# Optimization experiments

Measured on AMD Instinct MI355X. Metric: run time of the kernel, lower is better.

Reference implementation:

```python
import jax, jax.numpy as jnp
import numpy as np
from jax import lax

T, B, D, H = 512, 64, 256, 512  # time, batch, input_dim, hidden_dim


def setup_inputs() -> dict:
    key = jax.random.key(0)
    ks = jax.random.split(key, 9)
    fan_in = D + H
    s = 1.0 / np.sqrt(fan_in)
    inputs = jax.random.normal(ks[0], (T, B, D), dtype=jnp.float32)
    # torch nn.Linear weight layout: [out_features, in_features]
    Wf = jax.random.uniform(ks[1], (H, fan_in), jnp.float32, -s, s)
    bf = jax.random.uniform(ks[2], (H,), jnp.float32, -s, s)
    Wi = jax.random.uniform(ks[3], (H, fan_in), jnp.float32, -s, s)
    bi = jax.random.uniform(ks[4], (H,), jnp.float32, -s, s)
    Wg = jax.random.uniform(ks[5], (H, fan_in), jnp.float32, -s, s)
    bg = jax.random.uniform(ks[6], (H,), jnp.float32, -s, s)
    Wo = jax.random.uniform(ks[7], (H, fan_in), jnp.float32, -s, s)
    bo = jax.random.uniform(ks[8], (H,), jnp.float32, -s, s)
    return {"inputs": inputs, "Wf": Wf, "bf": bf, "Wi": Wi, "bi": bi,
            "Wg": Wg, "bg": bg, "Wo": Wo, "bo": bo}


def reference(inputs, Wf, bf, Wi, bi, Wg, bg, Wo, bo):
    # LSTM-style gated recurrence, n_qubits=0 path (no depth loop, proj_back = Identity)
    batch = inputs.shape[1]
    hidden = bf.shape[0]
    h0 = jnp.zeros((batch, hidden), inputs.dtype)
    c0 = jnp.zeros((batch, hidden), inputs.dtype)

    def step(carry, x):
        hx, cx = carry
        comb = jnp.concatenate([x, hx], axis=1)  # [B, D+H]
        f = jax.nn.sigmoid(comb @ Wf.T + bf)
        i = jax.nn.sigmoid(comb @ Wi.T + bi)
        g = jnp.tanh(comb @ Wg.T + bg)
        o = jax.nn.sigmoid(comb @ Wo.T + bo)
        cx = f * cx + i * g
        hx = o * jnp.tanh(cx)
        return (hx, cx), hx

    (hx, cx), outputs = lax.scan(step, (h0, c0), inputs)
    return outputs, hx, cx
```

## Files before the change

### kernel.cpp

```cpp
#include <hip/hip_runtime.h>
#include <stdint.h>

#define T_STEPS 512
#define BATCH   64
#define DIN     256
#define HID     512
#define KTOT    768
#define NTEAMS  4
#define TB      16
#define KK_X    8
#define KK_H    16
#define KK_ALL  24

#define POLL_BOUND (1 << 18)
#define DET_BOUND  (1 << 20)

typedef __bf16 v8bf __attribute__((ext_vector_type(8)));
typedef float  v4f  __attribute__((ext_vector_type(4)));
typedef unsigned int v4u __attribute__((ext_vector_type(4)));
typedef unsigned int v2u __attribute__((ext_vector_type(2)));

#define FLAGS_OFF 0
#define XCDB_OFF  8192
#define XCNT_OFF  8704
#define WPK_OFF   16384
#define XPK_OFF   (WPK_OFF + 3145728)
#define HBUF_OFF  (XPK_OFF + 16777216)
#define WS_NEED   ((size_t)HBUF_OFF + 33554432u)
#define FLAGS5_OFF 0
#define HBUF5_OFF  8192
#define WPK5_OFF   (HBUF5_OFF + 131072)
#define XPK5_OFF   (WPK5_OFF + 3145728)

#define LOADX4_DEV(d, a, IMM) \
  asm volatile("global_load_dwordx4 %0, %1, off offset:" IMM " sc1" \
               : "=v"(d) : "v"(a) : "memory")
#define LOADX4_PLAIN(d, a, IMM) \
  asm volatile("global_load_dwordx4 %0, %1, off offset:" IMM \
               : "=v"(d) : "v"(a) : "memory")
#define ST2_DEV(a, v) \
  asm volatile("global_store_dwordx2 %0, %1, off sc1" :: "v"(a), "v"(v) : "memory")
#define ST2_PLAIN(a, v) \
  asm volatile("global_store_dwordx2 %0, %1, off" :: "v"(a), "v"(v) : "memory")
#define ST_DW_DEV(a, v) \
  asm volatile("global_store_dword %0, %1, off sc1" :: "v"(a), "v"(v) : "memory")
#define ST_DW_SYS(a, v) \
  asm volatile("global_store_dword %0, %1, off sc0 sc1" :: "v"(a), "v"(v) : "memory")
#define LOADX4(d, a) \
  asm volatile("global_load_dwordx4 %0, %1, off" : "=v"(d) : "v"(a) : "memory")
#define LOAD_DW_NB(d, a) \
  asm volatile("global_load_dword %0, %1, off sc1" : "=v"(d) : "v"(a) : "memory")
#define WAIT1() asm volatile("s_waitcnt vmcnt(1)" ::: "memory")
#define DRAIN_VM() asm volatile("s_waitcnt vmcnt(0)" ::: "memory")

static __device__ __forceinline__ unsigned int ld_flag_dev(const unsigned int* p) {
  unsigned int v;
  asm volatile("global_load_dword %0, %1, off sc1\n\ts_waitcnt vmcnt(0)"
               : "=v"(v) : "v"(p) : "memory");
  return v;
}
static __device__ __forceinline__ unsigned int ld_dword_sys(const unsigned int* p) {
  unsigned int v;
  asm volatile("global_load_dword %0, %1, off sc0 sc1\n\ts_waitcnt vmcnt(0)"
               : "=v"(v) : "v"(p) : "memory");
  return v;
}

static __device__ __forceinline__ unsigned short f2bf(float x) {
  union { float f; uint32_t u; } v; v.f = x;
  uint32_t r = (v.u + 0x7fffu + ((v.u >> 16) & 1u)) >> 16;
  return (unsigned short)r;
}
static __device__ __forceinline__ float sigm(float x) {
  float e = __builtin_amdgcn_exp2f(-1.44269504f * x);
  return __builtin_amdgcn_rcpf(1.0f + e);
}
static __device__ __forceinline__ float tanh_(float x) {
  float e = __builtin_amdgcn_exp2f(2.88539008f * x);
  return 1.0f - 2.0f * __builtin_amdgcn_rcpf(e + 1.0f);
}

__global__ void pack_w(const float* __restrict__ Wf, const float* __restrict__ Wi,
                       const float* __restrict__ Wg, const float* __restrict__ Wo,
                       unsigned short* __restrict__ wpk) {
  int n = blockIdx.x * 256 + threadIdx.x;
  int l  = n & 63;
  int kk = (n >> 6) % KK_ALL;
  int wv = (n >> 6) / KK_ALL;
  int row  = l & 15;
  int gate = row & 3;
  int unit = (wv >> 2) * 16 + (wv & 3) * 4 + (row >> 2);
  int col  = kk * 32 + (l >> 4) * 8;
  const float* W = (gate == 0) ? Wf : (gate == 1) ? Wi : (gate == 2) ? Wg : Wo;
  const float* src = W + (size_t)unit * KTOT + col;
  unsigned short* dst = wpk + (size_t)n * 8;
#pragma unroll
  for (int e = 0; e < 8; e++) dst[e] = f2bf(src[e]);
}

__global__ void pack_x(const float* __restrict__ X, unsigned short* __restrict__ xpk) {
  int n = blockIdx.x * 256 + threadIdx.x;
  int l    = n & 63;
  int kk   = (n >> 6) & 7;
  int team = (n >> 9) & 3;
  int t    = n >> 11;
  int b    = team * TB + (l & 15);
  int col  = kk * 32 + (l >> 4) * 8;
  const float* src = X + ((size_t)(t * BATCH + b)) * DIN + col;
  unsigned short* dst = xpk + (size_t)n * 8;
#pragma unroll
  for (int e = 0; e < 8; e++) dst[e] = f2bf(src[e]);
}

__global__ void __launch_bounds__(256, 1)
lstm_mono(const float* __restrict__ bf_, const float* __restrict__ bi_,
          const float* __restrict__ bg_, const float* __restrict__ bo_,
          const unsigned short* __restrict__ wpk, const unsigned short* __restrict__ xpk,
          float* __restrict__ out, unsigned int* flags, unsigned int* xcdb,
          unsigned int* xcnt, unsigned short* hbuf) {
  int blk  = blockIdx.x;
  int team = blk & 7;
  if (team >= NTEAMS) return;
  int cu  = blk >> 3;
  int tid = threadIdx.x;
  int w   = tid >> 6, l = tid & 63;
  int brow = l & 15;
  int ul   = l >> 4;
  int u    = cu * 16 + w * 4 + ul;
  int bglob = team * TB + brow;

  __shared__ v4u hls[2048];
  __shared__ int mode_sh;

  {
    unsigned int* xb = xcdb + team * 32;
    unsigned int* xc = xcnt + team * 16;
    if (w == 0) {
      if (l == 0) {
        unsigned int myx;
        asm volatile("s_getreg_b32 %0, hwreg(HW_REG_XCC_ID)" : "=s"(myx));
        ST_DW_SYS(xb + cu, myx + 1u);
        DRAIN_VM();
        __hip_atomic_fetch_add(xc, 1u, __ATOMIC_RELEASE, __HIP_MEMORY_SCOPE_AGENT);
        int guard = 0;
        while (__hip_atomic_load(xc, __ATOMIC_ACQUIRE, __HIP_MEMORY_SCOPE_AGENT) < 32u) {
          if (++guard > DET_BOUND) break;
        }
      }
      unsigned int xv = ld_dword_sys(xb + (l & 31));
      int ok = (__all(xv == __shfl(xv, 0)) && __shfl(xv, 0) != 0u) ? 1 : 0;
      if (l == 0) mode_sh = ok;
    }
    __syncthreads();
  }
  const int fastsc = mode_sh;

  v4u wfu[KK_ALL];
  {
    const char* wp = (const char*)(wpk + ((size_t)(cu * 4 + w)) * (KK_ALL * 512) + l * 8);
#pragma unroll
    for (int kk = 0; kk < KK_ALL; kk++) LOADX4(wfu[kk], wp + (size_t)kk * 1024);
    DRAIN_VM();
  }
  float b0 = bf_[u], b1 = bi_[u], b2 = bg_[u], b3 = bo_[u];
  float c = 0.0f, hval = 0.0f;

  unsigned int* ftm = flags + (size_t)team * 32 * 16;
  unsigned int* myflag = ftm + (size_t)cu * 16;

  float* outb = out + (size_t)bglob * HID + u;

  for (int t = 0; t < T_STEPS; t++) {
    v8bf xf[KK_X];
    {
      const v8bf* xp = (const v8bf*)(xpk + ((size_t)(t * NTEAMS + team)) * (KK_X * 512) + l * 8);
#pragma unroll
      for (int kk = 0; kk < KK_X; kk++) xf[kk] = xp[kk * 64];
    }

    v4f acc[4];
    acc[0] = (v4f){b0, b1, b2, b3};
    acc[1] = (v4f){0.f, 0.f, 0.f, 0.f};
    acc[2] = (v4f){0.f, 0.f, 0.f, 0.f};
    acc[3] = (v4f){0.f, 0.f, 0.f, 0.f};
#pragma unroll
    for (int kk = 0; kk < KK_X; kk++)
      acc[kk & 3] = __builtin_amdgcn_mfma_f32_16x16x32_bf16(
          __builtin_bit_cast(v8bf, wfu[kk]), xf[kk], acc[kk & 3], 0, 0, 0);

    if (t > 0) {
      if (w == 0) {
        const unsigned int* pp = ftm + (size_t)(l & 31) * 16;
        unsigned int tg = (unsigned)t;
        unsigned int fa, fb;
        LOAD_DW_NB(fa, pp);
        int guard = 0;
        while (true) {
          LOAD_DW_NB(fb, pp);
          WAIT1();
          __builtin_amdgcn_sched_barrier(0);
          if (__all(fa >= tg)) break;
          LOAD_DW_NB(fa, pp);
          WAIT1();
          __builtin_amdgcn_sched_barrier(0);
          if (__all(fb >= tg)) break;
          if ((guard += 2) > POLL_BOUND) break;
        }
      }
      __syncthreads();

      const char* slab_t = (const char*)(hbuf + ((size_t)t * NTEAMS + team) * (TB * HID));
      const char* sb = slab_t + w * 4096 + l * 16;
      v4u s0, s1, s2, s3;
      if (fastsc) {
        LOADX4_PLAIN(s0, sb, "0");
        LOADX4_PLAIN(s1, sb, "1024");
        LOADX4_PLAIN(s2, sb, "2048");
        LOADX4_PLAIN(s3, sb, "3072");
      } else {
        LOADX4_DEV(s0, sb, "0");
        LOADX4_DEV(s1, sb, "1024");
        LOADX4_DEV(s2, sb, "2048");
        LOADX4_DEV(s3, sb, "3072");
      }
      DRAIN_VM();
      __builtin_amdgcn_sched_barrier(0);

      char* hl = (char*)hls + (t & 1) * 16384;
      {
        int r = w * 4;
        *(v4u*)(hl + (((r + 0) * 1024 + l * 16) ^ (((r + 0) & 7) << 4))) = s0;
        *(v4u*)(hl + (((r + 1) * 1024 + l * 16) ^ (((r + 1) & 7) << 4))) = s1;
        *(v4u*)(hl + (((r + 2) * 1024 + l * 16) ^ (((r + 2) & 7) << 4))) = s2;
        *(v4u*)(hl + (((r + 3) * 1024 + l * 16) ^ (((r + 3) & 7) << 4))) = s3;
      }
      __syncthreads();

#pragma unroll
      for (int kk = 0; kk < KK_H; kk++) {
        int off = (brow * 1024 + kk * 64 + ul * 16) ^ ((brow & 7) << 4);
        v8bf hf = *(const v8bf*)(hl + off);
        acc[kk & 3] = __builtin_amdgcn_mfma_f32_16x16x32_bf16(
            __builtin_bit_cast(v8bf, wfu[KK_X + kk]), hf, acc[kk & 3], 0, 0, 0);
      }
    }

    v4f g4 = (acc[0] + acc[1]) + (acc[2] + acc[3]);
    float fg = sigm(g4[0]);
    float ig = sigm(g4[1]);
    float gg = tanh_(g4[2]);
    float og = sigm(g4[3]);
    c    = fg * c + ig * gg;
    hval = og * tanh_(c);

    if (t < T_STEPS - 1) {
      float h0 = __shfl(hval, brow);
      float h1 = __shfl(hval, brow + 16);
      float h2 = __shfl(hval, brow + 32);
      float h3 = __shfl(hval, brow + 48);
      char* slab_n = (char*)(hbuf + ((size_t)(t + 1) * NTEAMS + team) * (TB * HID));
      if (l < 16) {
        v2u pk;
        pk.x = (unsigned)f2bf(h0) | ((unsigned)f2bf(h1) << 16);
        pk.y = (unsigned)f2bf(h2) | ((unsigned)f2bf(h3) << 16);
        char* pd = slab_n + brow * 1024 + cu * 32 + w * 8;
        if (fastsc) { ST2_PLAIN(pd, pk); } else { ST2_DEV(pd, pk); }
      }
      outb[(size_t)t * (BATCH * HID)] = hval;
      DRAIN_VM();
      __syncthreads();
      if (tid == 0) ST_DW_DEV(myflag, (unsigned)(t + 1));
    } else {
      outb[(size_t)t * (BATCH * HID)] = hval;
    }
  }

  float* hx = out + (size_t)T_STEPS * BATCH * HID;
  hx[(size_t)bglob * HID + u] = hval;
  float* cx = hx + BATCH * HID;
  cx[(size_t)bglob * HID + u] = c;
}

__global__ void __launch_bounds__(256, 1)
lstm_rec_r5(const float* __restrict__ bf_, const float* __restrict__ bi_,
            const float* __restrict__ bg_, const float* __restrict__ bo_,
            const unsigned short* __restrict__ wpk, const unsigned short* __restrict__ xpk,
            float* __restrict__ out, unsigned int* flags, unsigned short* hbuf) {
  int blk  = blockIdx.x;
  int team = blk & 7;
  if (team >= NTEAMS) return;
  int cu  = blk >> 3;
  int tid = threadIdx.x;
  int w   = tid >> 6, l = tid & 63;
  int brow = l & 15;
  int ul   = l >> 4;
  int u    = cu * 16 + w * 4 + ul;
  int bglob = team * TB + brow;

  __shared__ v4u hls[1024];
  char* hl = (char*)hls;

  v4u wfu[KK_ALL];
  {
    const char* wp = (const char*)(wpk + ((size_t)(cu * 4 + w)) * (KK_ALL * 512) + l * 8);
#pragma unroll
    for (int kk = 0; kk < KK_ALL; kk++) LOADX4(wfu[kk], wp + (size_t)kk * 1024);
    DRAIN_VM();
  }
  float b0 = bf_[u], b1 = bi_[u], b2 = bg_[u], b3 = bo_[u];
  float c = 0.0f, hval = 0.0f;

  char* slab0 = (char*)(hbuf + (size_t)team * 2 * (TB * HID));
  char* slab1 = slab0 + TB * HID * 2;
  unsigned int* ftm = flags + (size_t)team * 32 * 16;
  unsigned int* myflag = ftm + (size_t)cu * 16;
  float* outb = out + (size_t)bglob * HID + u;

  for (int t = 0; t < T_STEPS; t++) {
    v8bf xf[KK_X];
    {
      const v8bf* xp = (const v8bf*)(xpk + ((size_t)(t * NTEAMS + team)) * (KK_X * 512) + l * 8);
#pragma unroll
      for (int kk = 0; kk < KK_X; kk++) xf[kk] = xp[kk * 64];
    }
    if (t > 0) {
      if (w == 0) {
        const unsigned int* pp = ftm + (size_t)(l & 31) * 16;
        int guard = 0;
        while (true) {
          unsigned int v = ld_flag_dev(pp);
          if (__all(v >= (unsigned)t)) break;
          if (++guard > POLL_BOUND) break;
        }
      }
      __syncthreads();
    }
    v4u s0, s1, s2, s3;
    {
      const char* sb = ((t & 1) ? slab1 : slab0) + w * 4096 + l * 16;
      LOADX4_DEV(s0, sb, "0");
      LOADX4_DEV(s1, sb, "1024");
      LOADX4_DEV(s2, sb, "2048");
      LOADX4_DEV(s3, sb, "3072");
    }
    v4f acc[4];
    acc[0] = (v4f){b0, b1, b2, b3};
    acc[1] = (v4f){0.f, 0.f, 0.f, 0.f};
    acc[2] = (v4f){0.f, 0.f, 0.f, 0.f};
    acc[3] = (v4f){0.f, 0.f, 0.f, 0.f};
#pragma unroll
    for (int kk = 0; kk < KK_X; kk++)
      acc[kk & 3] = __builtin_amdgcn_mfma_f32_16x16x32_bf16(
          __builtin_bit_cast(v8bf, wfu[kk]), xf[kk], acc[kk & 3], 0, 0, 0);
    DRAIN_VM();
    __builtin_amdgcn_sched_barrier(0);
    {
      int r = w * 4;
      *(v4u*)(hl + (((r + 0) * 1024 + l * 16) ^ (((r + 0) & 7) << 4))) = s0;
      *(v4u*)(hl + (((r + 1) * 1024 + l * 16) ^ (((r + 1) & 7) << 4))) = s1;
      *(v4u*)(hl + (((r + 2) * 1024 + l * 16) ^ (((r + 2) & 7) << 4))) = s2;
      *(v4u*)(hl + (((r + 3) * 1024 + l * 16) ^ (((r + 3) & 7) << 4))) = s3;
    }
    __syncthreads();
#pragma unroll
    for (int kk = 0; kk < KK_H; kk++) {
      int off = (brow * 1024 + kk * 64 + ul * 16) ^ ((brow & 7) << 4);
      v8bf hf = *(const v8bf*)(hl + off);
      acc[kk & 3] = __builtin_amdgcn_mfma_f32_16x16x32_bf16(
          __builtin_bit_cast(v8bf, wfu[KK_X + kk]), hf, acc[kk & 3], 0, 0, 0);
    }
    v4f g4 = (acc[0] + acc[1]) + (acc[2] + acc[3]);
    float fg = sigm(g4[0]);
    float ig = sigm(g4[1]);
    float gg = tanh_(g4[2]);
    float og = sigm(g4[3]);
    c    = fg * c + ig * gg;
    hval = og * tanh_(c);
    if (t < T_STEPS - 1) {
      float h0 = __shfl(hval, brow);
      float h1 = __shfl(hval, brow + 16);
      float h2 = __shfl(hval, brow + 32);
      float h3 = __shfl(hval, brow + 48);
      if (l < 16) {
        v2u pk;
        pk.x = (unsigned)f2bf(h0) | ((unsigned)f2bf(h1) << 16);
        pk.y = (unsigned)f2bf(h2) | ((unsigned)f2bf(h3) << 16);
        char* pd = (((t + 1) & 1) ? slab1 : slab0) + brow * 1024 + cu * 32 + w * 8;
        ST2_DEV(pd, pk);
      }
      DRAIN_VM();
      __syncthreads();
      if (tid == 0) ST_DW_DEV(myflag, (unsigned)(t + 1));
    }
    outb[(size_t)t * (BATCH * HID)] = hval;
  }
  float* hx = out + (size_t)T_STEPS * BATCH * HID;
  hx[(size_t)bglob * HID + u] = hval;
  float* cx = hx + BATCH * HID;
  cx[(size_t)bglob * HID + u] = c;
}

extern "C" void kernel_launch(void* const* d_in, const int* in_sizes, int n_in,
                              void* d_out, int out_size, void* d_ws, size_t ws_size,
                              hipStream_t stream) {
  const float* X  = (const float*)d_in[0];
  const float* Wf = (const float*)d_in[1];
  const float* bf = (const float*)d_in[2];
  const float* Wi = (const float*)d_in[3];
  const float* bi = (const float*)d_in[4];
  const float* Wg = (const float*)d_in[5];
  const float* bg = (const float*)d_in[6];
  const float* Wo = (const float*)d_in[7];
  const float* bo = (const float*)d_in[8];
  float* out = (float*)d_out;
  char* ws = (char*)d_ws;

  if (ws_size >= WS_NEED) {
    unsigned int*   flags = (unsigned int*)(ws + FLAGS_OFF);
    unsigned int*   xcdb  = (unsigned int*)(ws + XCDB_OFF);
    unsigned int*   xcnt  = (unsigned int*)(ws + XCNT_OFF);
    unsigned short* wpk   = (unsigned short*)(ws + WPK_OFF);
    unsigned short* xpk   = (unsigned short*)(ws + XPK_OFF);
    unsigned short* hbuf  = (unsigned short*)(ws + HBUF_OFF);
    hipMemsetAsync(ws, 0, WPK_OFF, stream);
    pack_w<<<768, 256, 0, stream>>>(Wf, Wi, Wg, Wo, wpk);
    pack_x<<<4096, 256, 0, stream>>>(X, xpk);
    lstm_mono<<<256, 256, 0, stream>>>(bf, bi, bg, bo, wpk, xpk, out,
                                       flags, xcdb, xcnt, hbuf);
  } else {
    unsigned int*   flags = (unsigned int*)(ws + FLAGS5_OFF);
    unsigned short* hbuf  = (unsigned short*)(ws + HBUF5_OFF);
    unsigned short* wpk   = (unsigned short*)(ws + WPK5_OFF);
    unsigned short* xpk   = (unsigned short*)(ws + XPK5_OFF);
    hipMemsetAsync(ws, 0, WPK5_OFF, stream);
    pack_w<<<768, 256, 0, stream>>>(Wf, Wi, Wg, Wo, wpk);
    pack_x<<<4096, 256, 0, stream>>>(X, xpk);
    lstm_rec_r5<<<256, 256, 0, stream>>>(bf, bi, bg, bo, wpk, xpk, out, flags, hbuf);
  }
}
```

Before: 1.631 ms.

## Embed step tags in hidden-state words to replace flag polling with speculative loads

Each bf16 hidden value is now stored in a 32-bit word whose low 16 bits carry the step number. Readers issue the h loads speculatively before the x-part MFMAs, then check the tags and fall back to flag polling only if any word is stale. The h buffer becomes a 64-slot ring. The XCC-detection prologue and the plain-cache fast path are dropped in favour of device-scope loads and stores. This targets the poll-then-load round trip and the barrier on each step, at the cost of doubling the h traffic and relying on 16-byte stores being observed atomically.

```diff
diff --git a/kernel.cpp b/kernel.cpp
--- a/kernel.cpp
+++ b/kernel.cpp
@@ -13,7 +13,6 @@
 #define KK_ALL  24
 
 #define POLL_BOUND (1 << 18)
-#define DET_BOUND  (1 << 20)
 
 typedef __bf16 v8bf __attribute__((ext_vector_type(8)));
 typedef float  v4f  __attribute__((ext_vector_type(4)));
@@ -21,12 +20,10 @@
 typedef unsigned int v2u __attribute__((ext_vector_type(2)));
 
 #define FLAGS_OFF 0
-#define XCDB_OFF  8192
-#define XCNT_OFF  8704
 #define WPK_OFF   16384
 #define XPK_OFF   (WPK_OFF + 3145728)
-#define HBUF_OFF  (XPK_OFF + 16777216)
-#define WS_NEED   ((size_t)HBUF_OFF + 33554432u)
+#define HB32_OFF  (XPK_OFF + 16777216)
+#define WS_NEED   ((size_t)HB32_OFF + 8388608u)
 #define FLAGS5_OFF 0
 #define HBUF5_OFF  8192
 #define WPK5_OFF   (HBUF5_OFF + 131072)
@@ -35,33 +32,19 @@
 #define LOADX4_DEV(d, a, IMM) \
   asm volatile("global_load_dwordx4 %0, %1, off offset:" IMM " sc1" \
                : "=v"(d) : "v"(a) : "memory")
-#define LOADX4_PLAIN(d, a, IMM) \
-  asm volatile("global_load_dwordx4 %0, %1, off offset:" IMM \
-               : "=v"(d) : "v"(a) : "memory")
+#define ST4_DEV(a, v) \
+  asm volatile("global_store_dwordx4 %0, %1, off sc1" :: "v"(a), "v"(v) : "memory")
 #define ST2_DEV(a, v) \
   asm volatile("global_store_dwordx2 %0, %1, off sc1" :: "v"(a), "v"(v) : "memory")
-#define ST2_PLAIN(a, v) \
-  asm volatile("global_store_dwordx2 %0, %1, off" :: "v"(a), "v"(v) : "memory")
 #define ST_DW_DEV(a, v) \
   asm volatile("global_store_dword %0, %1, off sc1" :: "v"(a), "v"(v) : "memory")
-#define ST_DW_SYS(a, v) \
-  asm volatile("global_store_dword %0, %1, off sc0 sc1" :: "v"(a), "v"(v) : "memory")
 #define LOADX4(d, a) \
   asm volatile("global_load_dwordx4 %0, %1, off" : "=v"(d) : "v"(a) : "memory")
-#define LOAD_DW_NB(d, a) \
-  asm volatile("global_load_dword %0, %1, off sc1" : "=v"(d) : "v"(a) : "memory")
-#define WAIT1() asm volatile("s_waitcnt vmcnt(1)" ::: "memory")
 #define DRAIN_VM() asm volatile("s_waitcnt vmcnt(0)" ::: "memory")
 
 static __device__ __forceinline__ unsigned int ld_flag_dev(const unsigned int* p) {
   unsigned int v;
   asm volatile("global_load_dword %0, %1, off sc1\n\ts_waitcnt vmcnt(0)"
-               : "=v"(v) : "v"(p) : "memory");
-  return v;
-}
-static __device__ __forceinline__ unsigned int ld_dword_sys(const unsigned int* p) {
-  unsigned int v;
-  asm volatile("global_load_dword %0, %1, off sc0 sc1\n\ts_waitcnt vmcnt(0)"
                : "=v"(v) : "v"(p) : "memory");
   return v;
 }
@@ -113,11 +96,10 @@
 }
 
 __global__ void __launch_bounds__(256, 1)
-lstm_mono(const float* __restrict__ bf_, const float* __restrict__ bi_,
+lstm_spec(const float* __restrict__ bf_, const float* __restrict__ bi_,
           const float* __restrict__ bg_, const float* __restrict__ bo_,
           const unsigned short* __restrict__ wpk, const unsigned short* __restrict__ xpk,
-          float* __restrict__ out, unsigned int* flags, unsigned int* xcdb,
-          unsigned int* xcnt, unsigned short* hbuf) {
+          float* __restrict__ out, unsigned int* flags, unsigned int* hb32) {
   int blk  = blockIdx.x;
   int team = blk & 7;
   if (team >= NTEAMS) return;
@@ -130,30 +112,6 @@
   int bglob = team * TB + brow;
 
   __shared__ v4u hls[2048];
-  __shared__ int mode_sh;
-
-  {
-    unsigned int* xb = xcdb + team * 32;
-    unsigned int* xc = xcnt + team * 16;
-    if (w == 0) {
-      if (l == 0) {
-        unsigned int myx;
-        asm volatile("s_getreg_b32 %0, hwreg(HW_REG_XCC_ID)" : "=s"(myx));
-        ST_DW_SYS(xb + cu, myx + 1u);
-        DRAIN_VM();
-        __hip_atomic_fetch_add(xc, 1u, __ATOMIC_RELEASE, __HIP_MEMORY_SCOPE_AGENT);
-        int guard = 0;
-        while (__hip_atomic_load(xc, __ATOMIC_ACQUIRE, __HIP_MEMORY_SCOPE_AGENT) < 32u) {
-          if (++guard > DET_BOUND) break;
-        }
-      }
-      unsigned int xv = ld_dword_sys(xb + (l & 31));
-      int ok = (__all(xv == __shfl(xv, 0)) && __shfl(xv, 0) != 0u) ? 1 : 0;
-      if (l == 0) mode_sh = ok;
-    }
-    __syncthreads();
-  }
-  const int fastsc = mode_sh;
 
   v4u wfu[KK_ALL];
   {
@@ -168,16 +126,31 @@
   unsigned int* ftm = flags + (size_t)team * 32 * 16;
   unsigned int* myflag = ftm + (size_t)cu * 16;
 
+  int r    = w * 4 + (l >> 4);
+  int scol = l & 15;
+
   float* outb = out + (size_t)bglob * HID + u;
+  const unsigned int SEL = 0x07060302u;
 
   for (int t = 0; t < T_STEPS; t++) {
+    char* slab_t = (char*)(hb32 + ((size_t)(t & 63) * NTEAMS + team) * (TB * HID));
+    char* slab_n = (char*)(hb32 + ((size_t)((t + 1) & 63) * NTEAMS + team) * (TB * HID));
+
+    v4u p0, p1, p2, p3, p4, p5, p6, p7;
+    const char* sb = slab_t + r * 2048 + scol * 32;
+    if (t > 0) {
+      LOADX4_DEV(p0, sb, "0");    LOADX4_DEV(p1, sb, "16");
+      LOADX4_DEV(p2, sb, "512");  LOADX4_DEV(p3, sb, "528");
+      LOADX4_DEV(p4, sb, "1024"); LOADX4_DEV(p5, sb, "1040");
+      LOADX4_DEV(p6, sb, "1536"); LOADX4_DEV(p7, sb, "1552");
+    }
+
     v8bf xf[KK_X];
     {
       const v8bf* xp = (const v8bf*)(xpk + ((size_t)(t * NTEAMS + team)) * (KK_X * 512) + l * 8);
 #pragma unroll
       for (int kk = 0; kk < KK_X; kk++) xf[kk] = xp[kk * 64];
     }
-
     v4f acc[4];
     acc[0] = (v4f){b0, b1, b2, b3};
     acc[1] = (v4f){0.f, 0.f, 0.f, 0.f};
@@ -189,51 +162,62 @@
           __builtin_bit_cast(v8bf, wfu[kk]), xf[kk], acc[kk & 3], 0, 0, 0);
 
     if (t > 0) {
-      if (w == 0) {
+      DRAIN_VM();
+      __builtin_amdgcn_sched_barrier(0);
+
+      unsigned int tg = (unsigned)t;
+      unsigned int m;
+      m  = ((p0.x ^ tg) | (p0.y ^ tg) | (p0.z ^ tg) | (p0.w ^ tg));
+      m |= ((p1.x ^ tg) | (p1.y ^ tg) | (p1.z ^ tg) | (p1.w ^ tg));
+      m |= ((p2.x ^ tg) | (p2.y ^ tg) | (p2.z ^ tg) | (p2.w ^ tg));
+      m |= ((p3.x ^ tg) | (p3.y ^ tg) | (p3.z ^ tg) | (p3.w ^ tg));
+      m |= ((p4.x ^ tg) | (p4.y ^ tg) | (p4.z ^ tg) | (p4.w ^ tg));
+      m |= ((p5.x ^ tg) | (p5.y ^ tg) | (p5.z ^ tg) | (p5.w ^ tg));
+      m |= ((p6.x ^ tg) | (p6.y ^ tg) | (p6.z ^ tg) | (p6.w ^ tg));
+      m |= ((p7.x ^ tg) | (p7.y ^ tg) | (p7.z ^ tg) | (p7.w ^ tg));
+      m &= 0xFFFFu;
+      bool hit = __all(m == 0);
+
+      if (!hit) {
         const unsigned int* pp = ftm + (size_t)(l & 31) * 16;
-        unsigned int tg = (unsigned)t;
-        unsigned int fa, fb;
-        LOAD_DW_NB(fa, pp);
         int guard = 0;
         while (true) {
-          LOAD_DW_NB(fb, pp);
-          WAIT1();
-          __builtin_amdgcn_sched_barrier(0);
-          if (__all(fa >= tg)) break;
-          LOAD_DW_NB(fa, pp);
-          WAIT1();
-          __builtin_amdgcn_sched_barrier(0);
-          if (__all(fb >= tg)) break;
-          if ((guard += 2) > POLL_BOUND) break;
+          unsigned int v = ld_flag_dev(pp);
+          if (__all(v >= tg)) break;
+          if (++guard > POLL_BOUND) break;
         }
+        LOADX4_DEV(p0, sb, "0");    LOADX4_DEV(p1, sb, "16");
+        LOADX4_DEV(p2, sb, "512");  LOADX4_DEV(p3, sb, "528");
+        LOADX4_DEV(p4, sb, "1024"); LOADX4_DEV(p5, sb, "1040");
+        LOADX4_DEV(p6, sb, "1536"); LOADX4_DEV(p7, sb, "1552");
+        DRAIN_VM();
+        __builtin_amdgcn_sched_barrier(0);
       }
-      __syncthreads();
-
-      const char* slab_t = (const char*)(hbuf + ((size_t)t * NTEAMS + team) * (TB * HID));
-      const char* sb = slab_t + w * 4096 + l * 16;
-      v4u s0, s1, s2, s3;
-      if (fastsc) {
-        LOADX4_PLAIN(s0, sb, "0");
-        LOADX4_PLAIN(s1, sb, "1024");
-        LOADX4_PLAIN(s2, sb, "2048");
-        LOADX4_PLAIN(s3, sb, "3072");
-      } else {
-        LOADX4_DEV(s0, sb, "0");
-        LOADX4_DEV(s1, sb, "1024");
-        LOADX4_DEV(s2, sb, "2048");
-        LOADX4_DEV(s3, sb, "3072");
-      }
-      DRAIN_VM();
-      __builtin_amdgcn_sched_barrier(0);
 
       char* hl = (char*)hls + (t & 1) * 16384;
-      {
-        int r = w * 4;
-        *(v4u*)(hl + (((r + 0) * 1024 + l * 16) ^ (((r + 0) & 7) << 4))) = s0;
-        *(v4u*)(hl + (((r + 1) * 1024 + l * 16) ^ (((r + 1) & 7) << 4))) = s1;
-        *(v4u*)(hl + (((r + 2) * 1024 + l * 16) ^ (((r + 2) & 7) << 4))) = s2;
-        *(v4u*)(hl + (((r + 3) * 1024 + l * 16) ^ (((r + 3) & 7) << 4))) = s3;
-      }
+      int ob = r * 1024 + scol * 16;
+      int sz = (r & 7) << 4;
+      v4u o;
+      o.x = __builtin_amdgcn_perm(p0.y, p0.x, SEL);
+      o.y = __builtin_amdgcn_perm(p0.w, p0.z, SEL);
+      o.z = __builtin_amdgcn_perm(p1.y, p1.x, SEL);
+      o.w = __builtin_amdgcn_perm(p1.w, p1.z, SEL);
+      *(v4u*)(hl + ((ob + 0) ^ sz)) = o;
+      o.x = __builtin_amdgcn_perm(p2.y, p2.x, SEL);
+      o.y = __builtin_amdgcn_perm(p2.w, p2.z, SEL);
+      o.z = __builtin_amdgcn_perm(p3.y, p3.x, SEL);
+      o.w = __builtin_amdgcn_perm(p3.w, p3.z, SEL);
+      *(v4u*)(hl + ((ob + 256) ^ sz)) = o;
+      o.x = __builtin_amdgcn_perm(p4.y, p4.x, SEL);
+      o.y = __builtin_amdgcn_perm(p4.w, p4.z, SEL);
+      o.z = __builtin_amdgcn_perm(p5.y, p5.x, SEL);
+      o.w = __builtin_amdgcn_perm(p5.w, p5.z, SEL);
+      *(v4u*)(hl + ((ob + 512) ^ sz)) = o;
+      o.x = __builtin_amdgcn_perm(p6.y, p6.x, SEL);
+      o.y = __builtin_amdgcn_perm(p6.w, p6.z, SEL);
+      o.z = __builtin_amdgcn_perm(p7.y, p7.x, SEL);
+      o.w = __builtin_amdgcn_perm(p7.w, p7.z, SEL);
+      *(v4u*)(hl + ((ob + 768) ^ sz)) = o;
       __syncthreads();
 
 #pragma unroll
@@ -258,21 +242,21 @@
       float h1 = __shfl(hval, brow + 16);
       float h2 = __shfl(hval, brow + 32);
       float h3 = __shfl(hval, brow + 48);
-      char* slab_n = (char*)(hbuf + ((size_t)(t + 1) * NTEAMS + team) * (TB * HID));
       if (l < 16) {
-        v2u pk;
-        pk.x = (unsigned)f2bf(h0) | ((unsigned)f2bf(h1) << 16);
-        pk.y = (unsigned)f2bf(h2) | ((unsigned)f2bf(h3) << 16);
-        char* pd = slab_n + brow * 1024 + cu * 32 + w * 8;
-        if (fastsc) { ST2_PLAIN(pd, pk); } else { ST2_DEV(pd, pk); }
+        unsigned int tg1 = (unsigned)(t + 1);
+        v4u pk;
+        pk.x = ((unsigned)f2bf(h0) << 16) | tg1;
+        pk.y = ((unsigned)f2bf(h1) << 16) | tg1;
+        pk.z = ((unsigned)f2bf(h2) << 16) | tg1;
+        pk.w = ((unsigned)f2bf(h3) << 16) | tg1;
+        char* pd = slab_n + brow * 2048 + cu * 64 + w * 16;
+        ST4_DEV(pd, pk);
       }
-      outb[(size_t)t * (BATCH * HID)] = hval;
       DRAIN_VM();
       __syncthreads();
       if (tid == 0) ST_DW_DEV(myflag, (unsigned)(t + 1));
-    } else {
-      outb[(size_t)t * (BATCH * HID)] = hval;
-    }
+    }
+    outb[(size_t)t * (BATCH * HID)] = hval;
   }
 
   float* hx = out + (size_t)T_STEPS * BATCH * HID;
@@ -417,16 +401,14 @@
 
   if (ws_size >= WS_NEED) {
     unsigned int*   flags = (unsigned int*)(ws + FLAGS_OFF);
-    unsigned int*   xcdb  = (unsigned int*)(ws + XCDB_OFF);
-    unsigned int*   xcnt  = (unsigned int*)(ws + XCNT_OFF);
     unsigned short* wpk   = (unsigned short*)(ws + WPK_OFF);
     unsigned short* xpk   = (unsigned short*)(ws + XPK_OFF);
-    unsigned short* hbuf  = (unsigned short*)(ws + HBUF_OFF);
+    unsigned int*   hb32  = (unsigned int*)(ws + HB32_OFF);
     hipMemsetAsync(ws, 0, WPK_OFF, stream);
+    hipMemsetAsync(ws + HB32_OFF, 0, 8388608, stream);
     pack_w<<<768, 256, 0, stream>>>(Wf, Wi, Wg, Wo, wpk);
     pack_x<<<4096, 256, 0, stream>>>(X, xpk);
-    lstm_mono<<<256, 256, 0, stream>>>(bf, bi, bg, bo, wpk, xpk, out,
-                                       flags, xcdb, xcnt, hbuf);
+    lstm_spec<<<256, 256, 0, stream>>>(bf, bi, bg, bo, wpk, xpk, out, flags, hb32);
   } else {
     unsigned int*   flags = (unsigned int*)(ws + FLAGS5_OFF);
     unsigned short* hbuf  = (unsigned short*)(ws + HBUF5_OFF);
```

Result: faster. 1.466 ms (-10.1%).

## Poll flags via atomics, overlap x-MFMAs with h loads, defer output store

Applied to the files above, without the earlier changes.

Flag polling changes from double-buffered sc1 loads to a single atomic-add-of-zero read on the fast path, and the flag store becomes a plain store on that path. The input-projection MFMAs move from before the wait into the window where the h-slab loads are in flight, so they overlap memory latency instead of running ahead of the barrier. The output store now comes after the flag publish, which takes it off the critical path before the barrier. The atomic poll may cost more per iteration than the pipelined loads, and moving the x MFMAs after the wait could lengthen the critical path.

```diff
diff --git a/kernel.cpp b/kernel.cpp
--- a/kernel.cpp
+++ b/kernel.cpp
@@ -44,19 +44,24 @@
   asm volatile("global_store_dwordx2 %0, %1, off" :: "v"(a), "v"(v) : "memory")
 #define ST_DW_DEV(a, v) \
   asm volatile("global_store_dword %0, %1, off sc1" :: "v"(a), "v"(v) : "memory")
+#define ST_DW_PLAIN(a, v) \
+  asm volatile("global_store_dword %0, %1, off" :: "v"(a), "v"(v) : "memory")
 #define ST_DW_SYS(a, v) \
   asm volatile("global_store_dword %0, %1, off sc0 sc1" :: "v"(a), "v"(v) : "memory")
 #define LOADX4(d, a) \
   asm volatile("global_load_dwordx4 %0, %1, off" : "=v"(d) : "v"(a) : "memory")
-#define LOAD_DW_NB(d, a) \
-  asm volatile("global_load_dword %0, %1, off sc1" : "=v"(d) : "v"(a) : "memory")
-#define WAIT1() asm volatile("s_waitcnt vmcnt(1)" ::: "memory")
 #define DRAIN_VM() asm volatile("s_waitcnt vmcnt(0)" ::: "memory")
 
 static __device__ __forceinline__ unsigned int ld_flag_dev(const unsigned int* p) {
   unsigned int v;
   asm volatile("global_load_dword %0, %1, off sc1\n\ts_waitcnt vmcnt(0)"
                : "=v"(v) : "v"(p) : "memory");
+  return v;
+}
+static __device__ __forceinline__ unsigned int ld_flag_at(unsigned int* p) {
+  unsigned int v, z = 0u;
+  asm volatile("global_atomic_add %0, %1, %2, off sc0\n\ts_waitcnt vmcnt(0)"
+               : "=v"(v) : "v"(p), "v"(z) : "memory");
   return v;
 }
 static __device__ __forceinline__ unsigned int ld_dword_sys(const unsigned int* p) {
@@ -183,28 +188,16 @@
     acc[1] = (v4f){0.f, 0.f, 0.f, 0.f};
     acc[2] = (v4f){0.f, 0.f, 0.f, 0.f};
     acc[3] = (v4f){0.f, 0.f, 0.f, 0.f};
-#pragma unroll
-    for (int kk = 0; kk < KK_X; kk++)
-      acc[kk & 3] = __builtin_amdgcn_mfma_f32_16x16x32_bf16(
-          __builtin_bit_cast(v8bf, wfu[kk]), xf[kk], acc[kk & 3], 0, 0, 0);
 
     if (t > 0) {
       if (w == 0) {
-        const unsigned int* pp = ftm + (size_t)(l & 31) * 16;
+        unsigned int* pp = ftm + (size_t)(l & 31) * 16;
         unsigned int tg = (unsigned)t;
-        unsigned int fa, fb;
-        LOAD_DW_NB(fa, pp);
         int guard = 0;
         while (true) {
-          LOAD_DW_NB(fb, pp);
-          WAIT1();
-          __builtin_amdgcn_sched_barrier(0);
-          if (__all(fa >= tg)) break;
-          LOAD_DW_NB(fa, pp);
-          WAIT1();
-          __builtin_amdgcn_sched_barrier(0);
-          if (__all(fb >= tg)) break;
-          if ((guard += 2) > POLL_BOUND) break;
+          unsigned int v = fastsc ? ld_flag_at(pp) : ld_flag_dev((const unsigned int*)pp);
+          if (__all(v >= tg)) break;
+          if (++guard > POLL_BOUND) break;
         }
       }
       __syncthreads();
@@ -223,6 +216,12 @@
         LOADX4_DEV(s2, sb, "2048");
         LOADX4_DEV(s3, sb, "3072");
       }
+
+#pragma unroll
+      for (int kk = 0; kk < KK_X; kk++)
+        acc[kk & 3] = __builtin_amdgcn_mfma_f32_16x16x32_bf16(
+            __builtin_bit_cast(v8bf, wfu[kk]), xf[kk], acc[kk & 3], 0, 0, 0);
+
       DRAIN_VM();
       __builtin_amdgcn_sched_barrier(0);
 
@@ -243,6 +242,11 @@
         acc[kk & 3] = __builtin_amdgcn_mfma_f32_16x16x32_bf16(
             __builtin_bit_cast(v8bf, wfu[KK_X + kk]), hf, acc[kk & 3], 0, 0, 0);
       }
+    } else {
+#pragma unroll
+      for (int kk = 0; kk < KK_X; kk++)
+        acc[kk & 3] = __builtin_amdgcn_mfma_f32_16x16x32_bf16(
+            __builtin_bit_cast(v8bf, wfu[kk]), xf[kk], acc[kk & 3], 0, 0, 0);
     }
 
     v4f g4 = (acc[0] + acc[1]) + (acc[2] + acc[3]);
@@ -266,13 +270,14 @@
         char* pd = slab_n + brow * 1024 + cu * 32 + w * 8;
         if (fastsc) { ST2_PLAIN(pd, pk); } else { ST2_DEV(pd, pk); }
       }
-      outb[(size_t)t * (BATCH * HID)] = hval;
       DRAIN_VM();
       __syncthreads();
-      if (tid == 0) ST_DW_DEV(myflag, (unsigned)(t + 1));
-    } else {
-      outb[(size_t)t * (BATCH * HID)] = hval;
-    }
+      if (tid == 0) {
+        if (fastsc) { ST_DW_PLAIN(myflag, (unsigned)(t + 1)); }
+        else        { ST_DW_DEV(myflag, (unsigned)(t + 1)); }
+      }
+    }
+    outb[(size_t)t * (BATCH * HID)] = hval;
   }
 
   float* hx = out + (size_t)T_STEPS * BATCH * HID;
```

Result: slower. 2.312 ms (+41.7%).
